# Performance work log

Measured on AMD Instinct MI355X. Metric: run time of the kernel, lower is better.

The kernel has to match this reference:

```python
import jax, jax.numpy as jnp
import numpy as np

B, N, T, C = 2, 2048, 32, 32
NUM_BASES, MAX_K, K_CURR = 4, 32, 16


def setup_inputs() -> dict:
    key = jax.random.key(0)
    k1, k2, k3, k4, k5 = jax.random.split(key, 5)
    z = jax.random.normal(k1, (B, N, T, C), dtype=jnp.float32)
    neighbor_indices = jax.random.randint(k2, (N, K_CURR), 0, N)
    # parameters (match torch init scales)
    adjacency = 0.5 + 0.01 * jax.random.normal(k3, (N, MAX_K), dtype=jnp.float32)
    basis_weights = 0.02 * jax.random.normal(k4, (NUM_BASES, N, MAX_K), dtype=jnp.float32)
    channel_coeffs = jax.random.normal(k5, (C, NUM_BASES), dtype=jnp.float32)
    return {
        "z": z,
        "neighbor_indices": neighbor_indices,
        "adjacency": adjacency,
        "basis_weights": basis_weights,
        "channel_coeffs": channel_coeffs,
    }


def reference(z, neighbor_indices, adjacency, basis_weights, channel_coeffs):
    # z: [B,N,T,C], neighbor_indices: [N,k]
    k = neighbor_indices.shape[1]
    bases = basis_weights[:, :, :k]        # [num_bases, N, k]
    adj = adjacency[:, :k]                 # [N, k]
    # per-channel effective edge weights: [C, N, k]
    eff = jnp.einsum('cb,bnk->cnk', channel_coeffs, bases)
    edge_w = eff * adj[None, :, :]         # [C, N, k]
    w = jnp.transpose(edge_w, (1, 2, 0))   # [N, k, C]
    # gather neighbor features: [B, N, k, T, C]
    z_neigh = z[:, neighbor_indices]
    # weighted sum over neighbors, per-channel weights
    out = jnp.einsum('bnktc,nkc->bntc', z_neigh, w)
    return jnp.tanh(out)
```

## Files before the change

### kernel.cpp

```cpp
#include <hip/hip_runtime.h>


constexpr int BB_    = 2;
constexpr int NN_    = 2048;
constexpr int TT_    = 32;
constexpr int CC_    = 32;
constexpr int NBASE_ = 4;
constexpr int MAXK_  = 32;
constexpr int KC_    = 16;

constexpr int TQ_      = 4;
constexpr int SLICE_F4 = (TT_ / TQ_) * CC_ / 4;
constexpr int NODES_PB = 4;

__device__ __forceinline__ float fast_tanh(float x) {
    float e = __expf(2.0f * x);
    float r = __builtin_amdgcn_rcpf(e + 1.0f);
    return fmaf(-2.0f, r, 1.0f);
}

__global__ __launch_bounds__(256) void cgl_kernel(
    const float* __restrict__ z,
    const int*   __restrict__ nbr,
    const float* __restrict__ adj,
    const float* __restrict__ bw,
    const float* __restrict__ cc,
    float*       __restrict__ out)
{
    __shared__ __align__(16) float w_s[NODES_PB][KC_][CC_];
    __shared__ float bw_s[NODES_PB][NBASE_][KC_];
    __shared__ float cc_s[NBASE_ * CC_];
    __shared__ float adj_s[NODES_PB][KC_];
    __shared__ int   idx_s[NODES_PB][KC_];

    const int tid = threadIdx.x;
    const int blk = blockIdx.x;

    const int xcd   = blk & 7;
    const int b     = xcd >> 2;
    const int tq    = xcd & 3;
    const int group = blk >> 3;
    const int node0 = group * NODES_PB;

    {
        int nd = tid >> 6, bb = (tid >> 4) & 3, k = tid & 15;
        bw_s[nd][bb][k] = bw[((size_t)bb * NN_ + (node0 + nd)) * MAXK_ + k];

        if (tid < 64) {
            int nd2 = tid >> 4, k2 = tid & 15;
            adj_s[nd2][k2] = adj[(size_t)(node0 + nd2) * MAXK_ + k2];
        } else if (tid < 128) {
            int i = tid - 64, nd2 = i >> 4, k2 = i & 15;
            idx_s[nd2][k2] = nbr[(node0 + nd2) * KC_ + k2];
        } else {
            int i = tid - 128, bb2 = i >> 5, c2 = i & 31;
            cc_s[bb2 * CC_ + c2] = cc[c2 * NBASE_ + bb2];
        }
    }
    __syncthreads();

    {
        int i = tid;
        #pragma unroll
        for (int r = 0; r < 8; ++r, i += 256) {
            int nd = i >> 9, k = (i >> 5) & 15, c = i & 31;
            float s = cc_s[0 * CC_ + c] * bw_s[nd][0][k]
                    + cc_s[1 * CC_ + c] * bw_s[nd][1][k]
                    + cc_s[2 * CC_ + c] * bw_s[nd][2][k]
                    + cc_s[3 * CC_ + c] * bw_s[nd][3][k];
            w_s[nd][k][c] = s * adj_s[nd][k];
        }
    }
    __syncthreads();

    const int wave = tid >> 6;
    const int lane = tid & 63;
    const int n    = node0 + wave;
    const int c0   = (lane << 2) & 31;

    const float4* __restrict__ z4 = (const float4*)z;
    const size_t plane = (size_t)(TT_ * CC_ / 4);
    const size_t zb    = (size_t)b * NN_ * plane + (size_t)tq * SLICE_F4 + lane;

    float4 acc = make_float4(0.f, 0.f, 0.f, 0.f);
    #pragma unroll
    for (int k = 0; k < KC_; ++k) {
        const int nk = idx_s[wave][k];
        float4 zv = z4[zb + (size_t)nk * plane];
        float4 wv = *(const float4*)&w_s[wave][k][c0];
        acc.x = fmaf(zv.x, wv.x, acc.x);
        acc.y = fmaf(zv.y, wv.y, acc.y);
        acc.z = fmaf(zv.z, wv.z, acc.z);
        acc.w = fmaf(zv.w, wv.w, acc.w);
    }

    float4 o;
    o.x = fast_tanh(acc.x);
    o.y = fast_tanh(acc.y);
    o.z = fast_tanh(acc.z);
    o.w = fast_tanh(acc.w);

    ((float4*)out)[(size_t)b * NN_ * plane + (size_t)n * plane + tq * SLICE_F4 + lane] = o;
}

extern "C" void kernel_launch(void* const* d_in, const int* in_sizes, int n_in,
                              void* d_out, int out_size, void* d_ws, size_t ws_size,
                              hipStream_t stream) {
    const float* z   = (const float*)d_in[0];
    const int*   nbr = (const int*)d_in[1];
    const float* adj = (const float*)d_in[2];
    const float* bw  = (const float*)d_in[3];
    const float* cc  = (const float*)d_in[4];
    float* out = (float*)d_out;

    cgl_kernel<<<dim3(BB_ * TQ_ * (NN_ / NODES_PB)), dim3(256), 0, stream>>>(
        z, nbr, adj, bw, cc, out);
}
```

Measured before the change: 89.49 us.

## Convert z to bf16 in a pre-pass and prefetch neighbor rows into registers

A new kernel first converts z to bf16 in workspace memory. The gather kernel then reads half the bytes per neighbor row. The gather kernel also loads neighbor indices straight into uniform registers and issues all 16 neighbor loads before the weight-building barrier, so the loads overlap the weight computation. The cost is an extra full pass that reads z in fp32 and writes it in bf16, plus a loss of precision in the inputs.

Result: no change. 90.82 us (+1.5%).

```diff
diff --git a/kernel.cpp b/kernel.cpp
--- a/kernel.cpp
+++ b/kernel.cpp
@@ -10,8 +10,9 @@
 constexpr int KC_    = 16;
 
 constexpr int TQ_      = 4;
-constexpr int SLICE_F4 = (TT_ / TQ_) * CC_ / 4;
 constexpr int NODES_PB = 4;
+constexpr int PLANE_   = TT_ * CC_;
+constexpr int SLICE_   = (TT_ / TQ_) * CC_;
 
 __device__ __forceinline__ float fast_tanh(float x) {
     float e = __expf(2.0f * x);
@@ -19,8 +20,27 @@
     return fmaf(-2.0f, r, 1.0f);
 }
 
-__global__ __launch_bounds__(256) void cgl_kernel(
-    const float* __restrict__ z,
+__device__ __forceinline__ unsigned pack_bf16(float x, float y) {
+    unsigned ux = __float_as_uint(x), uy = __float_as_uint(y);
+    ux = (ux + 0x7fffu + ((ux >> 16) & 1u)) >> 16;
+    uy = (uy + 0x7fffu + ((uy >> 16) & 1u)) >> 16;
+    return ux | (uy << 16);
+}
+__device__ __forceinline__ float blo(unsigned u) { return __uint_as_float(u << 16); }
+__device__ __forceinline__ float bhi(unsigned u) { return __uint_as_float(u & 0xffff0000u); }
+
+__global__ __launch_bounds__(256) void z_to_bf16(
+    const float4* __restrict__ z4, uint4* __restrict__ zb)
+{
+    const int gid = blockIdx.x * 256 + threadIdx.x;
+    float4 a = z4[2 * gid];
+    float4 b = z4[2 * gid + 1];
+    zb[gid] = make_uint4(pack_bf16(a.x, a.y), pack_bf16(a.z, a.w),
+                         pack_bf16(b.x, b.y), pack_bf16(b.z, b.w));
+}
+
+__global__ __launch_bounds__(256, 4) void cgl_kernel(
+    const unsigned short* __restrict__ zb,
     const int*   __restrict__ nbr,
     const float* __restrict__ adj,
     const float* __restrict__ bw,
@@ -29,9 +49,8 @@
 {
     __shared__ __align__(16) float w_s[NODES_PB][KC_][CC_];
     __shared__ float bw_s[NODES_PB][NBASE_][KC_];
-    __shared__ float cc_s[NBASE_ * CC_];
+    __shared__ float cc_s[NBASE_][CC_];
     __shared__ float adj_s[NODES_PB][KC_];
-    __shared__ int   idx_s[NODES_PB][KC_];
 
     const int tid = threadIdx.x;
     const int blk = blockIdx.x;
@@ -49,14 +68,21 @@
         if (tid < 64) {
             int nd2 = tid >> 4, k2 = tid & 15;
             adj_s[nd2][k2] = adj[(size_t)(node0 + nd2) * MAXK_ + k2];
-        } else if (tid < 128) {
-            int i = tid - 64, nd2 = i >> 4, k2 = i & 15;
-            idx_s[nd2][k2] = nbr[(node0 + nd2) * KC_ + k2];
-        } else {
-            int i = tid - 128, bb2 = i >> 5, c2 = i & 31;
-            cc_s[bb2 * CC_ + c2] = cc[c2 * NBASE_ + bb2];
+        } else if (tid < 192) {
+            int i = tid - 64, bb2 = i >> 5, c2 = i & 31;
+            cc_s[bb2][c2] = cc[c2 * NBASE_ + bb2];
         }
     }
+
+    const int wave = tid >> 6;
+    const int lane = tid & 63;
+    const int n    = node0 + wave;
+    const int* __restrict__ ip = nbr + n * KC_;
+    int nks[KC_];
+    #pragma unroll
+    for (int k = 0; k < KC_; ++k)
+        nks[k] = __builtin_amdgcn_readfirstlane(ip[k]);
+
     __syncthreads();
 
     {
@@ -64,34 +90,35 @@
         #pragma unroll
         for (int r = 0; r < 8; ++r, i += 256) {
             int nd = i >> 9, k = (i >> 5) & 15, c = i & 31;
-            float s = cc_s[0 * CC_ + c] * bw_s[nd][0][k]
-                    + cc_s[1 * CC_ + c] * bw_s[nd][1][k]
-                    + cc_s[2 * CC_ + c] * bw_s[nd][2][k]
-                    + cc_s[3 * CC_ + c] * bw_s[nd][3][k];
+            float s = cc_s[0][c] * bw_s[nd][0][k]
+                    + cc_s[1][c] * bw_s[nd][1][k]
+                    + cc_s[2][c] * bw_s[nd][2][k]
+                    + cc_s[3][c] * bw_s[nd][3][k];
             w_s[nd][k][c] = s * adj_s[nd][k];
         }
     }
+
+    uint2 zv[KC_];
+    {
+        const size_t sbase = (size_t)b * NN_ * PLANE_ + (size_t)tq * SLICE_;
+        #pragma unroll
+        for (int k = 0; k < KC_; ++k) {
+            const unsigned short* row = zb + sbase + (size_t)nks[k] * PLANE_;
+            zv[k] = ((const uint2*)row)[lane];
+        }
+    }
+
     __syncthreads();
 
-    const int wave = tid >> 6;
-    const int lane = tid & 63;
-    const int n    = node0 + wave;
-    const int c0   = (lane << 2) & 31;
-
-    const float4* __restrict__ z4 = (const float4*)z;
-    const size_t plane = (size_t)(TT_ * CC_ / 4);
-    const size_t zb    = (size_t)b * NN_ * plane + (size_t)tq * SLICE_F4 + lane;
-
+    const int c0 = (lane & 7) << 2;
     float4 acc = make_float4(0.f, 0.f, 0.f, 0.f);
     #pragma unroll
     for (int k = 0; k < KC_; ++k) {
-        const int nk = idx_s[wave][k];
-        float4 zv = z4[zb + (size_t)nk * plane];
         float4 wv = *(const float4*)&w_s[wave][k][c0];
-        acc.x = fmaf(zv.x, wv.x, acc.x);
-        acc.y = fmaf(zv.y, wv.y, acc.y);
-        acc.z = fmaf(zv.z, wv.z, acc.z);
-        acc.w = fmaf(zv.w, wv.w, acc.w);
+        acc.x = fmaf(blo(zv[k].x), wv.x, acc.x);
+        acc.y = fmaf(bhi(zv[k].x), wv.y, acc.y);
+        acc.z = fmaf(blo(zv[k].y), wv.z, acc.z);
+        acc.w = fmaf(bhi(zv[k].y), wv.w, acc.w);
     }
 
     float4 o;
@@ -100,7 +127,8 @@
     o.z = fast_tanh(acc.z);
     o.w = fast_tanh(acc.w);
 
-    ((float4*)out)[(size_t)b * NN_ * plane + (size_t)n * plane + tq * SLICE_F4 + lane] = o;
+    float* op = out + ((size_t)(b * NN_ + n) * TT_ + tq * (TT_ / TQ_)) * CC_;
+    ((float4*)op)[lane] = o;
 }
 
 extern "C" void kernel_launch(void* const* d_in, const int* in_sizes, int n_in,
@@ -112,7 +140,10 @@
     const float* bw  = (const float*)d_in[3];
     const float* cc  = (const float*)d_in[4];
     float* out = (float*)d_out;
+    unsigned short* zb16 = (unsigned short*)d_ws;
 
+    z_to_bf16<<<dim3(BB_ * NN_ * PLANE_ / 8 / 256), dim3(256), 0, stream>>>(
+        (const float4*)z, (uint4*)zb16);
     cgl_kernel<<<dim3(BB_ * TQ_ * (NN_ / NODES_PB)), dim3(256), 0, stream>>>(
-        z, nbr, adj, bw, cc, out);
+        zb16, nbr, adj, bw, cc, out);
 }
```
